# Performance work log

Measured on AMD Instinct MI355X. Metric: run time of the kernel, lower is better.

Reference implementation:

```python
import jax, jax.numpy as jnp
import numpy as np


def setup_inputs() -> dict:
    key = jax.random.key(0)
    k1, k2 = jax.random.split(key)
    B, N, M, D = 8, 8192, 8192, 3
    gts = jax.random.normal(k1, (B, N, D), dtype=jnp.float32)
    preds = jax.random.normal(k2, (B, M, D), dtype=jnp.float32)
    return {"gts": gts, "preds": preds}


def reference(gts, preds):
    # Chamfer distance (pytorch3d defaults): squared L2, mean over points,
    # mean over batch, sum of both directions.
    x2 = jnp.sum(gts * gts, axis=-1)          # [B, N]
    y2 = jnp.sum(preds * preds, axis=-1)      # [B, M]
    xy = jnp.einsum('bnd,bmd->bnm', gts, preds)  # [B, N, M]
    d2 = x2[:, :, None] + y2[:, None, :] - 2.0 * xy
    d2 = jnp.maximum(d2, 0.0)  # guard tiny negative values from cancellation
    cham_x = jnp.mean(jnp.min(d2, axis=2))  # x -> nearest y, mean over N then B
    cham_y = jnp.mean(jnp.min(d2, axis=1))  # y -> nearest x, mean over M then B
    return cham_x + cham_y
```

## Files before the change

### kernel.cpp

```cpp
#include <hip/hip_runtime.h>
#include <hip/hip_bf16.h>
#include <math.h>


#define BLOCK 256
#define WAVES 4
#define QPW 64
#define NCHUNK 2

typedef short short8 __attribute__((ext_vector_type(8)));
typedef float f32x16 __attribute__((ext_vector_type(16)));

union U16S { uint4 v; short8 s; };

__device__ __forceinline__ unsigned int bf16hi(float f) {
    __hip_bfloat16 h = __float2bfloat16(f);
    return (unsigned int)*reinterpret_cast<unsigned short*>(&h);
}
__device__ __forceinline__ float bf16f(unsigned int u) {
    unsigned short us = (unsigned short)u;
    __hip_bfloat16 h;
    *reinterpret_cast<unsigned short*>(&h) = us;
    return __bfloat162float(h);
}

__device__ __forceinline__ f32x16 mfma_bf16(short8 a, short8 b, f32x16 c) {
    f32x16 d;
    asm volatile("v_mfma_f32_32x32x16_bf16 %0, %1, %2, %3"
                 : "=v"(d) : "v"(a), "v"(b), "v"(c));
    return d;
}
__device__ __forceinline__ void mfma_fence4(f32x16& a, f32x16& b, f32x16& c, f32x16& d) {
    asm volatile("s_nop 7\n\ts_nop 7" : "+v"(a), "+v"(b), "+v"(c), "+v"(d));
}

__global__ void prep_kernel(const float* __restrict__ gts, const float* __restrict__ preds,
                            int nG, int nP, uint4* __restrict__ recG, uint4* __restrict__ recP,
                            float* __restrict__ q2, float* out) {
    const int t = blockIdx.x * blockDim.x + threadIdx.x;
    if (t == 0) out[0] = 0.0f;
    const int i0 = t * 4;
    if (i0 >= nG + nP) return;
    const float* src;
    uint4* rec;
    if (i0 < nG) { src = gts + 3 * (size_t)i0;                rec = recG + i0; }
    else         { src = preds + 3 * (size_t)(i0 - nG);       rec = recP + (i0 - nG); }
    const float4 f0 = ((const float4*)src)[0];
    const float4 f1 = ((const float4*)src)[1];
    const float4 f2 = ((const float4*)src)[2];
    const float xs[4] = {f0.x, f0.w, f1.z, f2.y};
    const float ys[4] = {f0.y, f1.x, f1.w, f2.z};
    const float zs[4] = {f0.z, f1.y, f2.x, f2.w};
    float4 q2v;
    #pragma unroll
    for (int i = 0; i < 4; ++i) {
        const float x = xs[i], y = ys[i], z = zs[i];
        const float n2 = x * x + y * y + z * z;
        ((float*)&q2v)[i] = n2;
        const float w = -0.5f * n2;
        const unsigned int xh = bf16hi(x), yh = bf16hi(y), zh = bf16hi(z), wh = bf16hi(w);
        const unsigned int xl = bf16hi(x - bf16f(xh));
        const unsigned int yl = bf16hi(y - bf16f(yh));
        const unsigned int zl = bf16hi(z - bf16f(zh));
        const unsigned int wl = bf16hi(w - bf16f(wh));
        rec[i] = make_uint4(xh | (yh << 16), zh | (wh << 16),
                            xl | (yl << 16), zl | (wl << 16));
    }
    ((float4*)q2)[t] = q2v;
}

__global__ void __launch_bounds__(BLOCK, 3)
nn_kernel(const uint4* __restrict__ recG, const uint4* __restrict__ recP,
          float* __restrict__ kpart, int N, int M, int B) {
    const int z = blockIdx.z;
    const bool dirX = (z < B);
    const int b = dirX ? z : z - B;
    const int NQ = dirX ? N : M;
    const int NR = dirX ? M : N;
    const uint4* Qr = (dirX ? recG : recP) + (size_t)b * NQ;
    const uint4* Rr = (dirX ? recP : recG) + (size_t)b * NR;
    const int nGP = B * N + B * M;
    float* outK = kpart + (size_t)blockIdx.y * nGP + (dirX ? 0 : B * N) + (size_t)b * NQ;

    const int tid = threadIdx.x;
    const int lane = tid & 63;
    const int wave = tid >> 6;
    const int m = lane & 31;
    const bool hiK = lane >= 32;
    const int qBase = (blockIdx.x * WAVES + wave) * QPW;

    const uint4 q0 = Qr[qBase + m];
    const uint4 q1 = Qr[qBase + 32 + m];
    U16S a;
    a.v.x = hiK ? q0.z : q0.x;
    a.v.y = hiK ? (q0.w & 0xFFFFu) : ((q0.y & 0xFFFFu) | 0x3F800000u);
    a.v.z = hiK ? 0u : a.v.x;
    a.v.w = hiK ? 0u : a.v.y;
    const short8 A0 = a.s;
    a.v.x = hiK ? q1.z : q1.x;
    a.v.y = hiK ? (q1.w & 0xFFFFu) : ((q1.y & 0xFFFFu) | 0x3F800000u);
    a.v.z = hiK ? 0u : a.v.x;
    a.v.w = hiK ? 0u : a.v.y;
    const short8 A1 = a.s;

    f32x16 zc;
    #pragma unroll
    for (int r = 0; r < 16; ++r) zc[r] = 0.0f;
    f32x16 k0, k1;
    #pragma unroll
    for (int r = 0; r < 16; ++r) { k0[r] = -INFINITY; k1[r] = -INFINITY; }

    const int chunk = NR / NCHUNK;
    const uint4* p = Rr + (size_t)blockIdx.y * chunk + m;
    const int iters = chunk / 64;

    uint4 t0 = p[0], t1 = p[32];
    #pragma unroll 1
    for (int it = 0; it < iters; ++it) {
        const uint4 n0 = p[64];
        const uint4 n1 = p[96];

        U16S b0, b1;
        b0.v = t0; b1.v = t1;
        f32x16 c0 = mfma_bf16(A0, b0.s, zc);
        f32x16 c1 = mfma_bf16(A1, b0.s, zc);
        f32x16 c2 = mfma_bf16(A0, b1.s, zc);
        f32x16 c3 = mfma_bf16(A1, b1.s, zc);
        mfma_fence4(c0, c1, c2, c3);
        #pragma unroll
        for (int r = 0; r < 16; ++r) {
            k0[r] = fmaxf(fmaxf(c0[r], c2[r]), k0[r]);
            k1[r] = fmaxf(fmaxf(c1[r], c3[r]), k1[r]);
        }

        t0 = n0; t1 = n1;
        p += 64;
    }

    __shared__ float sT[WAVES][64][36];
    #pragma unroll
    for (int r = 0; r < 16; ++r) {
        const int row = (r & 3) + 8 * (r >> 2) + 4 * (lane >> 5);
        sT[wave][row][m]      = k0[r];
        sT[wave][32 + row][m] = k1[r];
    }
    const float4* rowp = (const float4*)&sT[wave][lane][0];
    float4 m01 = rowp[0];
    #pragma unroll
    for (int kk = 1; kk < 8; ++kk) {
        const float4 tt = rowp[kk];
        m01.x = fmaxf(m01.x, tt.x); m01.y = fmaxf(m01.y, tt.y);
        m01.z = fmaxf(m01.z, tt.z); m01.w = fmaxf(m01.w, tt.w);
    }
    const float cmax = fmaxf(fmaxf(m01.x, m01.y), fmaxf(m01.z, m01.w));
    outK[qBase + lane] = cmax;
}

__global__ void __launch_bounds__(BLOCK)
reduce_kernel(const float* __restrict__ kpart, const float* __restrict__ q2,
              int nG, int nP, float invx, float invy, float* __restrict__ out) {
    const int total = nG + nP;
    float local = 0.0f;
    for (int idx = blockIdx.x * blockDim.x + threadIdx.x; idx < total;
         idx += gridDim.x * blockDim.x) {
        const float c = fmaxf(kpart[idx], kpart[total + idx]);
        const float inv = (idx < nG) ? invx : invy;
        local += fmaxf(q2[idx] - 2.0f * c, 0.0f) * inv;
    }
    __shared__ float waveSums[BLOCK / 64];
    float v = local;
    #pragma unroll
    for (int off = 32; off; off >>= 1) v += __shfl_xor(v, off);
    if ((threadIdx.x & 63) == 0) waveSums[threadIdx.x >> 6] = v;
    __syncthreads();
    if (threadIdx.x == 0) {
        float s = 0.0f;
        #pragma unroll
        for (int w = 0; w < BLOCK / 64; ++w) s += waveSums[w];
        atomicAdd(out, s);
    }
}

extern "C" void kernel_launch(void* const* d_in, const int* in_sizes, int n_in,
                              void* d_out, int out_size, void* d_ws, size_t ws_size,
                              hipStream_t stream) {
    const float* gts   = (const float*)d_in[0];
    const float* preds = (const float*)d_in[1];
    float* out = (float*)d_out;

    const int B = 8;
    const int N = in_sizes[0] / (B * 3);
    const int M = in_sizes[1] / (B * 3);
    const int nG = B * N, nP = B * M;

    uint4* recG  = (uint4*)d_ws;
    uint4* recP  = recG + nG;
    float* q2    = (float*)(recP + nP);
    float* kpart = q2 + (nG + nP);

    prep_kernel<<<((nG + nP) / 4 + BLOCK - 1) / BLOCK, BLOCK, 0, stream>>>(
        gts, preds, nG, nP, recG, recP, q2, out);

    dim3 grid(N / (WAVES * QPW), NCHUNK, 2 * B);
    nn_kernel<<<grid, BLOCK, 0, stream>>>(recG, recP, kpart, N, M, B);

    reduce_kernel<<<256, BLOCK, 0, stream>>>(
        kpart, q2, nG, nP, 1.0f / (float)nG, 1.0f / (float)nP, out);
}
```

Baseline: 103.3 us.

## Halve queries per wave, split reference records across K-halves, drop asm MFMA fences

```diff
diff --git a/kernel.cpp b/kernel.cpp
--- a/kernel.cpp
+++ b/kernel.cpp
@@ -5,7 +5,7 @@
 
 #define BLOCK 256
 #define WAVES 4
-#define QPW 64
+#define QPW 32
 #define NCHUNK 2
 
 typedef short short8 __attribute__((ext_vector_type(8)));
@@ -22,16 +22,6 @@
     __hip_bfloat16 h;
     *reinterpret_cast<unsigned short*>(&h) = us;
     return __bfloat162float(h);
-}
-
-__device__ __forceinline__ f32x16 mfma_bf16(short8 a, short8 b, f32x16 c) {
-    f32x16 d;
-    asm volatile("v_mfma_f32_32x32x16_bf16 %0, %1, %2, %3"
-                 : "=v"(d) : "v"(a), "v"(b), "v"(c));
-    return d;
-}
-__device__ __forceinline__ void mfma_fence4(f32x16& a, f32x16& b, f32x16& c, f32x16& d) {
-    asm volatile("s_nop 7\n\ts_nop 7" : "+v"(a), "+v"(b), "+v"(c), "+v"(d));
 }
 
 __global__ void prep_kernel(const float* __restrict__ gts, const float* __restrict__ preds,
@@ -69,7 +59,7 @@
     ((float4*)q2)[t] = q2v;
 }
 
-__global__ void __launch_bounds__(BLOCK, 3)
+__global__ void __launch_bounds__(BLOCK, 5)
 nn_kernel(const uint4* __restrict__ recG, const uint4* __restrict__ recP,
           float* __restrict__ kpart, int N, int M, int B) {
     const int z = blockIdx.z;
@@ -90,70 +80,72 @@
     const int qBase = (blockIdx.x * WAVES + wave) * QPW;
 
     const uint4 q0 = Qr[qBase + m];
-    const uint4 q1 = Qr[qBase + 32 + m];
     U16S a;
-    a.v.x = hiK ? q0.z : q0.x;
-    a.v.y = hiK ? (q0.w & 0xFFFFu) : ((q0.y & 0xFFFFu) | 0x3F800000u);
-    a.v.z = hiK ? 0u : a.v.x;
-    a.v.w = hiK ? 0u : a.v.y;
-    const short8 A0 = a.s;
-    a.v.x = hiK ? q1.z : q1.x;
-    a.v.y = hiK ? (q1.w & 0xFFFFu) : ((q1.y & 0xFFFFu) | 0x3F800000u);
-    a.v.z = hiK ? 0u : a.v.x;
-    a.v.w = hiK ? 0u : a.v.y;
-    const short8 A1 = a.s;
-
-    f32x16 zc;
-    #pragma unroll
-    for (int r = 0; r < 16; ++r) zc[r] = 0.0f;
-    f32x16 k0, k1;
-    #pragma unroll
-    for (int r = 0; r < 16; ++r) { k0[r] = -INFINITY; k1[r] = -INFINITY; }
+    a.v.x = q0.x;
+    a.v.y = (q0.y & 0xFFFFu) | 0x3F800000u;
+    a.v.z = hiK ? 0u : q0.z;
+    a.v.w = hiK ? 0u : (q0.w & 0xFFFFu);
+    const short8 A = a.s;
+
+    const f32x16 zc = (f32x16)0.0f;
+    f32x16 k;
+    #pragma unroll
+    for (int r = 0; r < 16; ++r) k[r] = -INFINITY;
 
     const int chunk = NR / NCHUNK;
-    const uint4* p = Rr + (size_t)blockIdx.y * chunk + m;
+    const uint2* p = (const uint2*)(Rr + (size_t)blockIdx.y * chunk) + 2 * m + (hiK ? 1 : 0);
     const int iters = chunk / 64;
 
-    uint4 t0 = p[0], t1 = p[32];
+    uint2 t0 = p[0], t1 = p[64];
     #pragma unroll 1
-    for (int it = 0; it < iters; ++it) {
-        const uint4 n0 = p[64];
-        const uint4 n1 = p[96];
-
-        U16S b0, b1;
-        b0.v = t0; b1.v = t1;
-        f32x16 c0 = mfma_bf16(A0, b0.s, zc);
-        f32x16 c1 = mfma_bf16(A1, b0.s, zc);
-        f32x16 c2 = mfma_bf16(A0, b1.s, zc);
-        f32x16 c3 = mfma_bf16(A1, b1.s, zc);
-        mfma_fence4(c0, c1, c2, c3);
-        #pragma unroll
-        for (int r = 0; r < 16; ++r) {
-            k0[r] = fmaxf(fmaxf(c0[r], c2[r]), k0[r]);
-            k1[r] = fmaxf(fmaxf(c1[r], c3[r]), k1[r]);
+    for (int it = 0; it < iters; it += 2) {
+        uint2 n0 = p[128], n1 = p[192];
+        {
+            U16S b0, b1;
+            b0.v.x = t0.x; b0.v.y = t0.y;
+            b0.v.z = hiK ? 0u : t0.x; b0.v.w = hiK ? 0u : t0.y;
+            b1.v.x = t1.x; b1.v.y = t1.y;
+            b1.v.z = hiK ? 0u : t1.x; b1.v.w = hiK ? 0u : t1.y;
+            const f32x16 c0 = __builtin_amdgcn_mfma_f32_32x32x16_bf16(A, b0.s, zc, 0, 0, 0);
+            const f32x16 c1 = __builtin_amdgcn_mfma_f32_32x32x16_bf16(A, b1.s, zc, 0, 0, 0);
+            #pragma unroll
+            for (int r = 0; r < 16; ++r)
+                k[r] = fmaxf(fmaxf(c0[r], c1[r]), k[r]);
         }
-
-        t0 = n0; t1 = n1;
-        p += 64;
-    }
-
-    __shared__ float sT[WAVES][64][36];
+        t0 = p[256]; t1 = p[320];
+        {
+            U16S b0, b1;
+            b0.v.x = n0.x; b0.v.y = n0.y;
+            b0.v.z = hiK ? 0u : n0.x; b0.v.w = hiK ? 0u : n0.y;
+            b1.v.x = n1.x; b1.v.y = n1.y;
+            b1.v.z = hiK ? 0u : n1.x; b1.v.w = hiK ? 0u : n1.y;
+            const f32x16 c0 = __builtin_amdgcn_mfma_f32_32x32x16_bf16(A, b0.s, zc, 0, 0, 0);
+            const f32x16 c1 = __builtin_amdgcn_mfma_f32_32x32x16_bf16(A, b1.s, zc, 0, 0, 0);
+            #pragma unroll
+            for (int r = 0; r < 16; ++r)
+                k[r] = fmaxf(fmaxf(c0[r], c1[r]), k[r]);
+        }
+        p += 256;
+    }
+
+    __shared__ float sT[WAVES][32][36];
     #pragma unroll
     for (int r = 0; r < 16; ++r) {
         const int row = (r & 3) + 8 * (r >> 2) + 4 * (lane >> 5);
-        sT[wave][row][m]      = k0[r];
-        sT[wave][32 + row][m] = k1[r];
-    }
-    const float4* rowp = (const float4*)&sT[wave][lane][0];
-    float4 m01 = rowp[0];
-    #pragma unroll
-    for (int kk = 1; kk < 8; ++kk) {
-        const float4 tt = rowp[kk];
-        m01.x = fmaxf(m01.x, tt.x); m01.y = fmaxf(m01.y, tt.y);
-        m01.z = fmaxf(m01.z, tt.z); m01.w = fmaxf(m01.w, tt.w);
-    }
-    const float cmax = fmaxf(fmaxf(m01.x, m01.y), fmaxf(m01.z, m01.w));
-    outK[qBase + lane] = cmax;
+        sT[wave][row][m] = k[r];
+    }
+    if (lane < 32) {
+        const float4* rowp = (const float4*)&sT[wave][lane][0];
+        float4 m01 = rowp[0];
+        #pragma unroll
+        for (int kk = 1; kk < 8; ++kk) {
+            const float4 tt = rowp[kk];
+            m01.x = fmaxf(m01.x, tt.x); m01.y = fmaxf(m01.y, tt.y);
+            m01.z = fmaxf(m01.z, tt.z); m01.w = fmaxf(m01.w, tt.w);
+        }
+        const float cmax = fmaxf(fmaxf(m01.x, m01.y), fmaxf(m01.z, m01.w));
+        outK[qBase + lane] = cmax;
+    }
 }
 
 __global__ void __launch_bounds__(BLOCK)
```

Measured after the change: 105.4 us. 1.02x slower.
